# Kernel tuning notes

Hardware: AMD Instinct MI355X
Metric: run time of the kernel (lower is better)

The kernel has to match this reference:

```python
import jax, jax.numpy as jnp
import numpy as np

HIDDEN = 1024
HEADS = 16
HEAD_DIM = HIDDEN // HEADS


def setup_inputs() -> dict:
    key = jax.random.key(0)
    ks = jax.random.split(key, 11)
    B, S = 2, 2048
    s = 1.0 / np.sqrt(HIDDEN)
    return {
        "query": jax.random.normal(ks[0], (B, S, HIDDEN), jnp.float32),
        "key": jax.random.normal(ks[1], (B, S, HIDDEN), jnp.float32),
        "value": jax.random.normal(ks[2], (B, S, HIDDEN), jnp.float32),
        "Wq": jax.random.uniform(ks[3], (HIDDEN, HIDDEN), jnp.float32, -s, s),
        "bq": jax.random.uniform(ks[4], (HIDDEN,), jnp.float32, -s, s),
        "Wk": jax.random.uniform(ks[5], (HIDDEN, HIDDEN), jnp.float32, -s, s),
        "bk": jax.random.uniform(ks[6], (HIDDEN,), jnp.float32, -s, s),
        "Wv": jax.random.uniform(ks[7], (HIDDEN, HIDDEN), jnp.float32, -s, s),
        "bv": jax.random.uniform(ks[8], (HIDDEN,), jnp.float32, -s, s),
        "Wo": jax.random.uniform(ks[9], (HIDDEN, HIDDEN), jnp.float32, -s, s),
        "bo": jax.random.uniform(ks[10], (HIDDEN,), jnp.float32, -s, s),
    }


def reference(query, key, value, Wq, bq, Wk, bk, Wv, bv, Wo, bo):
    B, Sq, _ = query.shape
    Sk = key.shape[1]
    # projections (torch Linear: x @ W^T + b)
    Q = (query @ Wq.T + bq).reshape(B, Sq, HEADS, HEAD_DIM).transpose(0, 2, 1, 3)
    K = (key @ Wk.T + bk).reshape(B, Sk, HEADS, HEAD_DIM).transpose(0, 2, 1, 3)
    V = (value @ Wv.T + bv).reshape(B, Sk, HEADS, HEAD_DIM).transpose(0, 2, 1, 3)
    scale = jnp.sqrt(jnp.float32(HEAD_DIM))
    scores = jnp.einsum("bhqd,bhkd->bhqk", Q, K) / scale  # [B,H,Sq,Sk]
    # causal mask (is_causal=True, Sq>1)
    causal = jnp.tril(jnp.ones((Sq, Sk), dtype=bool))
    scores = jnp.where(causal[None, None], scores, -jnp.inf)
    attn = jax.nn.softmax(scores, axis=-1)
    out = jnp.einsum("bhqk,bhkd->bhqd", attn, V)
    out = out.transpose(0, 2, 1, 3).reshape(B, Sq, HIDDEN)
    return out @ Wo.T + bo
```

## Files before the change

### kernel.cpp

```cpp
#include <hip/hip_runtime.h>
#include <hip/hip_bf16.h>


typedef __attribute__((ext_vector_type(4))) float f32x4;
typedef __attribute__((ext_vector_type(8))) short bf16x8;
typedef unsigned short u16;

#define SEQ   2048
#define NH    16
#define HD    64
#define HID   1024
#define CEXP  0.1803368801f
#define MEG   1048576u

static __device__ __forceinline__ u16 f2bf(float f) {
  union { __hip_bfloat16 h; u16 u; } c;
  c.h = __float2bfloat16(f);
  return c.u;
}

static __device__ __forceinline__ int swz(int row, int col8) {
  return col8 ^ ((row & 7) << 3);
}

static __device__ __forceinline__ void gll16(const void* g, void* l) {
  __builtin_amdgcn_global_load_lds(
      (const __attribute__((address_space(1))) void*)g,
      (__attribute__((address_space(3))) void*)l, 16, 0, 0);
}

__global__ __launch_bounds__(256) void cvt_kernel(
    const float* __restrict__ Wq, const float* __restrict__ Wk,
    const float* __restrict__ Wv, const float* __restrict__ Wo,
    const float* __restrict__ q, const float* __restrict__ k,
    const float* __restrict__ v,
    u16* __restrict__ wsout, u16* __restrict__ dob) {
  const int y = blockIdx.y;
  const int c = y & 3;
  const float* src;
  u16* dst;
  if (y < 4) {
    src = (y == 0) ? Wq : (y == 1) ? Wk : (y == 2) ? Wv : Wo;
    dst = wsout + (size_t)y * MEG;
  } else if (y < 8) {
    src = q + (size_t)c * MEG;
    dst = wsout + 4u * MEG + (size_t)c * MEG;
  } else if (y < 12) {
    src = k + (size_t)c * MEG;
    dst = dob + (size_t)c * MEG;
  } else {
    src = v + (size_t)c * MEG;
    dst = dob + 4u * MEG + (size_t)c * MEG;
  }
  int i = (blockIdx.x * 256 + threadIdx.x) * 4;
  float4 f = *(const float4*)(src + i);
  ushort4 o;
  o.x = f2bf(f.x); o.y = f2bf(f.y); o.z = f2bf(f.z); o.w = f2bf(f.w);
  *(ushort4*)(dst + i) = o;
}

__global__ __launch_bounds__(256) void proj_kernel(
    const u16* __restrict__ Xq, const u16* __restrict__ Xk,
    const u16* __restrict__ Xv, const u16* __restrict__ Wc,
    const float* __restrict__ bq, const float* __restrict__ bk,
    const float* __restrict__ bvp,
    u16* __restrict__ Qo, u16* __restrict__ Ko, u16* __restrict__ Vto) {
  __shared__ u16 As[2][128 * 64];
  __shared__ u16 Bs[2][128 * 64];

  const int tid  = threadIdx.x;
  const int lane = tid & 63;
  const int wid  = tid >> 6;
  const int wm   = wid >> 1, wn = wid & 1;
  const int l15  = lane & 15;
  const int lhi  = lane >> 4;
  const int z    = blockIdx.z;
  const int bm   = blockIdx.x * 128;
  const int bn   = blockIdx.y * 128;

  const u16* X = (z == 0) ? Xq : (z == 1) ? Xk : Xv;
  const u16* W = Wc + (size_t)z * (HID * HID);
  const float* bias = (z == 0) ? bq : (z == 1) ? bk : bvp;

  f32x4 acc[4][4];
#pragma unroll
  for (int i = 0; i < 4; i++)
#pragma unroll
    for (int j = 0; j < 4; j++) acc[i][j] = (f32x4){0.f, 0.f, 0.f, 0.f};

  const int lrow  = lane >> 3;
  const int gcol8 = lane & 7;

#define PROJ_STAGE(buf, k0)                                                       \
  {                                                                               \
    _Pragma("unroll")                                                             \
    for (int c = 0; c < 4; c++) {                                                 \
      const int row  = c * 32 + wid * 8 + lrow;                                   \
      const int scol = (gcol8 ^ (row & 7)) * 8;      \
      gll16(X + (size_t)(bm + row) * HID + (k0) + scol,                           \
            (char*)&As[buf][0] + c * 4096 + wid * 1024);                          \
      gll16(W + (size_t)(bn + row) * HID + (k0) + scol,                           \
            (char*)&Bs[buf][0] + c * 4096 + wid * 1024);                          \
    }                                                                             \
  }

  PROJ_STAGE(0, 0);
  for (int t = 0; t < 16; t++) {
    __syncthreads();
    if (t < 15) PROJ_STAGE((t + 1) & 1, (t + 1) * 64);
    const u16* A = &As[t & 1][0];
    const u16* B = &Bs[t & 1][0];
#pragma unroll
    for (int ks = 0; ks < 2; ks++) {
      bf16x8 af[4], bfm[4];
#pragma unroll
      for (int i = 0; i < 4; i++) {
        const int row = wm * 64 + i * 16 + l15;
        af[i] = *(const bf16x8*)&A[row * 64 + swz(row, ks * 32 + lhi * 8)];
      }
#pragma unroll
      for (int j = 0; j < 4; j++) {
        const int row = wn * 64 + j * 16 + l15;
        bfm[j] = *(const bf16x8*)&B[row * 64 + swz(row, ks * 32 + lhi * 8)];
      }
#pragma unroll
      for (int i = 0; i < 4; i++)
#pragma unroll
        for (int j = 0; j < 4; j++)
          acc[i][j] = __builtin_amdgcn_mfma_f32_16x16x32_bf16(af[i], bfm[j], acc[i][j], 0, 0, 0);
    }
  }

  const int bb = bm >> 11;
#pragma unroll
  for (int j = 0; j < 4; j++) {
    const int n = bn + wn * 64 + j * 16 + l15;
    const float bv_ = bias[n];
    const int h = n >> 6, d = n & 63;
    if (z == 2) {
#pragma unroll
      for (int i = 0; i < 4; i++) {
        const int s0 = (bm + wm * 64 + i * 16 + lhi * 4) & 2047;
        ushort4 t;
        t.x = f2bf(acc[i][j][0] + bv_);
        t.y = f2bf(acc[i][j][1] + bv_);
        t.z = f2bf(acc[i][j][2] + bv_);
        t.w = f2bf(acc[i][j][3] + bv_);
        *(ushort4*)&Vto[((size_t)(bb * NH + h) * HD + d) * SEQ + s0] = t;
      }
    } else {
      u16* O = z ? Ko : Qo;
#pragma unroll
      for (int i = 0; i < 4; i++)
#pragma unroll
        for (int r = 0; r < 4; r++) {
          const int m = bm + wm * 64 + i * 16 + lhi * 4 + r;
          const int s = m & 2047;
          O[(((size_t)(bb * NH + h) * SEQ + s) << 6) + d] = f2bf(acc[i][j][r] + bv_);
        }
    }
  }
#undef PROJ_STAGE
}

__global__ __launch_bounds__(512) void attn_kernel(
    const u16* __restrict__ Q, const u16* __restrict__ K,
    const u16* __restrict__ Vt, u16* __restrict__ Aout) {
  __shared__ __align__(16) char pool[51200];

  const int tid  = threadIdx.x;
  const int lane = tid & 63;
  const int wid  = tid >> 6;
  const int rw   = wid & 3;
  const int g    = wid >> 2;
  const int l15  = lane & 15;
  const int lhi  = lane >> 4;

  const int flat = blockIdx.x;
  const int slot = flat >> 3;
  const int bh   = (flat & 7) * 4 + (slot & 3);
  const int qt   = 31 - (slot >> 2);
  const int b    = bh >> 4, h = bh & 15;
  const size_t base = (size_t)bh * SEQ * HD;

  u16* Ksh = (u16*)(pool + g * 8192);
  u16* Vsh = (u16*)(pool + 16384 + g * 8192);
  u16* Psh = (u16*)(pool + 32768 + wid * 2304);

  const int qrow = qt * 64 + rw * 16 + l15;
  bf16x8 aq[2];
  aq[0] = *(const bf16x8*)&Q[base + (size_t)qrow * HD + lhi * 8];
  aq[1] = *(const bf16x8*)&Q[base + (size_t)qrow * HD + 32 + lhi * 8];

  f32x4 o[4];
#pragma unroll
  for (int n = 0; n < 4; n++) o[n] = (f32x4){0.f, 0.f, 0.f, 0.f};
  float m_s = -1e30f, l_s = 0.f;

  const int gt   = tid & 255;
  const int srow = gt >> 2;
  const int sd   = (gt & 3) * 16;

  bf16x8 pk0, pk1, pv0, pv1;

#define ATTN_LOAD(kt_)                                                            \
  {                                                                               \
    const u16* kp = K + base + (size_t)((kt_) * 64 + srow) * HD + sd;             \
    pk0 = *(const bf16x8*)kp;                                                     \
    pk1 = *(const bf16x8*)(kp + 8);                                               \
    const u16* vp = Vt + base + (size_t)srow * SEQ + (kt_) * 64 + sd;             \
    pv0 = *(const bf16x8*)vp;                                                     \
    pv1 = *(const bf16x8*)(vp + 8);                                               \
  }

  if (g <= qt) ATTN_LOAD(g);

  const int nsteps = qt / 2 + 1;
  for (int it = 0; it < nsteps; ++it) {
    const int kt = 2 * it + g;
    const bool act = (kt <= qt);
    __syncthreads();
    if (act) {
      *(bf16x8*)&Ksh[srow * 64 + swz(srow, sd)]     = pk0;
      *(bf16x8*)&Ksh[srow * 64 + swz(srow, sd + 8)] = pk1;
      *(bf16x8*)&Vsh[srow * 64 + swz(srow, sd)]     = pv0;
      *(bf16x8*)&Vsh[srow * 64 + swz(srow, sd + 8)] = pv1;
    }
    const int ktn = kt + 2;
    if (ktn <= qt) ATTN_LOAD(ktn);
    __syncthreads();
    if (act) {
      f32x4 sc[4];
      __builtin_amdgcn_s_setprio(1);
#pragma unroll
      for (int n = 0; n < 4; n++) {
        sc[n] = (f32x4){0.f, 0.f, 0.f, 0.f};
#pragma unroll
        for (int ks = 0; ks < 2; ks++) {
          const int krow = n * 16 + l15;
          bf16x8 bk = *(const bf16x8*)&Ksh[krow * 64 + swz(krow, ks * 32 + lhi * 8)];
          sc[n] = __builtin_amdgcn_mfma_f32_16x16x32_bf16(bk, aq[ks], sc[n], 0, 0, 0);
        }
      }
      __builtin_amdgcn_s_setprio(0);
      if (kt == qt) {
#pragma unroll
        for (int n = 0; n < 4; n++)
#pragma unroll
          for (int r = 0; r < 4; r++)
            if (kt * 64 + n * 16 + lhi * 4 + r > qrow) sc[n][r] = -1e30f;
      }
      float mx = -1e30f;
#pragma unroll
      for (int n = 0; n < 4; n++)
        mx = fmaxf(mx, fmaxf(fmaxf(sc[n][0], sc[n][1]), fmaxf(sc[n][2], sc[n][3])));
      mx = fmaxf(mx, __shfl_xor(mx, 16, 64));
      mx = fmaxf(mx, __shfl_xor(mx, 32, 64));
      if (__any(mx > m_s + 64.0f)) {
        const float mnew = fmaxf(m_s, mx);
        const float fac = __builtin_amdgcn_exp2f((m_s - mnew) * CEXP);
        l_s *= fac;
        m_s = mnew;
        float facr[4];
#pragma unroll
        for (int r = 0; r < 4; r++) facr[r] = __shfl(fac, lhi * 4 + r, 64);
#pragma unroll
        for (int n = 0; n < 4; n++) {
          o[n][0] *= facr[0]; o[n][1] *= facr[1];
          o[n][2] *= facr[2]; o[n][3] *= facr[3];
        }
      }
      const float nmc = -m_s * CEXP;
      float ps = 0.f;
      u16 pb[4][4];
#pragma unroll
      for (int n = 0; n < 4; n++)
#pragma unroll
        for (int r = 0; r < 4; r++) {
          const float e = __builtin_amdgcn_exp2f(fmaf(sc[n][r], CEXP, nmc));
          ps += e;
          pb[n][r] = f2bf(e);
        }
      ps += __shfl_xor(ps, 16, 64);
      ps += __shfl_xor(ps, 32, 64);
      l_s += ps;
#pragma unroll
      for (int n = 0; n < 4; n++) {
        ushort4 t; t.x = pb[n][0]; t.y = pb[n][1]; t.z = pb[n][2]; t.w = pb[n][3];
        *(ushort4*)&Psh[l15 * 72 + n * 16 + lhi * 4] = t;
      }
      bf16x8 ap0 = *(const bf16x8*)&Psh[l15 * 72 + lhi * 8];
      bf16x8 ap1 = *(const bf16x8*)&Psh[l15 * 72 + 32 + lhi * 8];
      __builtin_amdgcn_s_setprio(1);
#pragma unroll
      for (int n = 0; n < 4; n++) {
        const int vrow = n * 16 + l15;
        bf16x8 bv0 = *(const bf16x8*)&Vsh[vrow * 64 + swz(vrow, lhi * 8)];
        bf16x8 bv1 = *(const bf16x8*)&Vsh[vrow * 64 + swz(vrow, 32 + lhi * 8)];
        o[n] = __builtin_amdgcn_mfma_f32_16x16x32_bf16(ap0, bv0, o[n], 0, 0, 0);
        o[n] = __builtin_amdgcn_mfma_f32_16x16x32_bf16(ap1, bv1, o[n], 0, 0, 0);
      }
      __builtin_amdgcn_s_setprio(0);
    }
  }
#undef ATTN_LOAD

  __syncthreads();
  float m_o[4], l_o[4];
#pragma unroll
  for (int r = 0; r < 4; r++) {
    m_o[r] = __shfl(m_s, lhi * 4 + r, 64);
    l_o[r] = __shfl(l_s, lhi * 4 + r, 64);
  }

  f32x4* comb = (f32x4*)pool;
  const int ci = (rw * 64 + lane) * 6;
  if (g == 0) {
#pragma unroll
    for (int n = 0; n < 4; n++) comb[ci + n] = o[n];
    comb[ci + 4] = (f32x4){m_o[0], m_o[1], m_o[2], m_o[3]};
    comb[ci + 5] = (f32x4){l_o[0], l_o[1], l_o[2], l_o[3]};
  }
  __syncthreads();
  if (g == 1) {
    f32x4 m0 = comb[ci + 4];
    f32x4 l0 = comb[ci + 5];
    float a0[4], a1[4], inv[4];
#pragma unroll
    for (int r = 0; r < 4; r++) {
      const float m = fmaxf(m0[r], m_o[r]);
      a0[r] = __builtin_amdgcn_exp2f((m0[r] - m) * CEXP);
      a1[r] = __builtin_amdgcn_exp2f((m_o[r] - m) * CEXP);
      inv[r] = 1.0f / (l0[r] * a0[r] + l_o[r] * a1[r]);
    }
#pragma unroll
    for (int n = 0; n < 4; n++) {
      f32x4 o0 = comb[ci + n];
#pragma unroll
      for (int r = 0; r < 4; r++) {
        const int rowg = qt * 64 + rw * 16 + lhi * 4 + r;
        const float val = (o0[r] * a0[r] + o[n][r] * a1[r]) * inv[r];
        Aout[(((size_t)(b * SEQ + rowg)) << 10) + h * 64 + n * 16 + l15] = f2bf(val);
      }
    }
  }
}

__global__ __launch_bounds__(256) void oproj_kernel(
    const u16* __restrict__ X, const u16* __restrict__ W,
    const float* __restrict__ bias, float* __restrict__ Out) {
  __shared__ u16 As[2][128 * 64];
  __shared__ u16 Bs[2][64 * 64];

  const int tid  = threadIdx.x;
  const int lane = tid & 63;
  const int wid  = tid >> 6;
  const int wm   = wid >> 1, wn = wid & 1;
  const int l15  = lane & 15;
  const int lhi  = lane >> 4;
  const int bm   = blockIdx.x * 128;
  const int bn   = blockIdx.y * 64;

  f32x4 acc[4][2];
#pragma unroll
  for (int i = 0; i < 4; i++)
#pragma unroll
    for (int j = 0; j < 2; j++) acc[i][j] = (f32x4){0.f, 0.f, 0.f, 0.f};

  const int lrow  = lane >> 3;
  const int gcol8 = lane & 7;

#define OPROJ_STAGE(buf, k0)                                                      \
  {                                                                               \
    _Pragma("unroll")                                                             \
    for (int c = 0; c < 4; c++) {                                                 \
      const int row  = c * 32 + wid * 8 + lrow;                                   \
      const int scol = (gcol8 ^ (row & 7)) * 8;                                   \
      gll16(X + (size_t)(bm + row) * HID + (k0) + scol,                           \
            (char*)&As[buf][0] + c * 4096 + wid * 1024);                          \
      if (c < 2)                                                                  \
        gll16(W + (size_t)(bn + row) * HID + (k0) + scol,                         \
              (char*)&Bs[buf][0] + c * 4096 + wid * 1024);                        \
    }                                                                             \
  }

  OPROJ_STAGE(0, 0);
  for (int t = 0; t < 16; t++) {
    __syncthreads();
    if (t < 15) OPROJ_STAGE((t + 1) & 1, (t + 1) * 64);
    const u16* A = &As[t & 1][0];
    const u16* B = &Bs[t & 1][0];
#pragma unroll
    for (int ks = 0; ks < 2; ks++) {
      bf16x8 af[4], bfm[2];
#pragma unroll
      for (int i = 0; i < 4; i++) {
        const int row = wm * 64 + i * 16 + l15;
        af[i] = *(const bf16x8*)&A[row * 64 + swz(row, ks * 32 + lhi * 8)];
      }
#pragma unroll
      for (int j = 0; j < 2; j++) {
        const int row = wn * 32 + j * 16 + l15;
        bfm[j] = *(const bf16x8*)&B[row * 64 + swz(row, ks * 32 + lhi * 8)];
      }
#pragma unroll
      for (int i = 0; i < 4; i++)
#pragma unroll
        for (int j = 0; j < 2; j++)
          acc[i][j] = __builtin_amdgcn_mfma_f32_16x16x32_bf16(af[i], bfm[j], acc[i][j], 0, 0, 0);
    }
  }
#undef OPROJ_STAGE

#pragma unroll
  for (int j = 0; j < 2; j++) {
    const int n = bn + wn * 32 + j * 16 + l15;
    const float bv_ = bias[n];
#pragma unroll
    for (int i = 0; i < 4; i++)
#pragma unroll
      for (int r = 0; r < 4; r++) {
        const int m = bm + wm * 64 + i * 16 + lhi * 4 + r;
        Out[(size_t)m * HID + n] = acc[i][j][r] + bv_;
      }
  }
}

extern "C" void kernel_launch(void* const* d_in, const int* in_sizes, int n_in,
                              void* d_out, int out_size, void* d_ws, size_t ws_size,
                              hipStream_t stream) {
  const float* q  = (const float*)d_in[0];
  const float* k  = (const float*)d_in[1];
  const float* v  = (const float*)d_in[2];
  const float* Wq = (const float*)d_in[3];
  const float* bq = (const float*)d_in[4];
  const float* Wk = (const float*)d_in[5];
  const float* bk = (const float*)d_in[6];
  const float* Wv = (const float*)d_in[7];
  const float* bv = (const float*)d_in[8];
  const float* Wo = (const float*)d_in[9];
  const float* bo = (const float*)d_in[10];

  u16* ws   = (u16*)d_ws;
  u16* wqkv = ws;
  u16* wob  = ws + 3u * MEG;
  u16* qb   = ws + 4u * MEG;
  u16* Qb   = ws + 8u * MEG;
  u16* Kb   = ws + 12u * MEG;
  u16* Vtb  = ws + 16u * MEG;
  u16* Ab   = qb;
  u16* kbf  = (u16*)d_out;
  u16* vbf  = (u16*)d_out + 4u * MEG;

  cvt_kernel<<<dim3(1024, 16), 256, 0, stream>>>(Wq, Wk, Wv, Wo, q, k, v, ws, kbf);

  proj_kernel<<<dim3(32, 8, 3), 256, 0, stream>>>(qb, kbf, vbf, wqkv, bq, bk, bv,
                                                  Qb, Kb, Vtb);

  attn_kernel<<<dim3(1024), 512, 0, stream>>>(Qb, Kb, Vtb, Ab);

  oproj_kernel<<<dim3(32, 16), 256, 0, stream>>>(Ab, wob, bo, (float*)d_out);
}
```

Before: 119.6 us.

## Replace __syncthreads with raw barriers and explicit partial vmcnt waits

After: 112.8 us. -5.8%, faster.

```diff
diff --git a/kernel.cpp b/kernel.cpp
--- a/kernel.cpp
+++ b/kernel.cpp
@@ -12,6 +12,9 @@
 #define HID   1024
 #define CEXP  0.1803368801f
 #define MEG   1048576u
+
+#define BAR()  __builtin_amdgcn_s_barrier()
+#define SCHED0() __builtin_amdgcn_sched_barrier(0)
 
 static __device__ __forceinline__ u16 f2bf(float f) {
   union { __hip_bfloat16 h; u16 u; } c;
@@ -106,8 +109,15 @@
 
   PROJ_STAGE(0, 0);
   for (int t = 0; t < 16; t++) {
-    __syncthreads();
-    if (t < 15) PROJ_STAGE((t + 1) & 1, (t + 1) * 64);
+    BAR();
+    if (t < 15) {
+      PROJ_STAGE((t + 1) & 1, (t + 1) * 64);
+      asm volatile("s_waitcnt vmcnt(8)" ::: "memory");
+    } else {
+      asm volatile("s_waitcnt vmcnt(0)" ::: "memory");
+    }
+    BAR();
+    SCHED0();
     const u16* A = &As[t & 1][0];
     const u16* B = &Bs[t & 1][0];
 #pragma unroll
@@ -130,6 +140,7 @@
           acc[i][j] = __builtin_amdgcn_mfma_f32_16x16x32_bf16(af[i], bfm[j], acc[i][j], 0, 0, 0);
     }
   }
+#undef PROJ_STAGE
 
   const int bb = bm >> 11;
 #pragma unroll
@@ -160,7 +171,6 @@
         }
     }
   }
-#undef PROJ_STAGE
 }
 
 __global__ __launch_bounds__(512) void attn_kernel(
@@ -219,7 +229,7 @@
   for (int it = 0; it < nsteps; ++it) {
     const int kt = 2 * it + g;
     const bool act = (kt <= qt);
-    __syncthreads();
+    BAR();
     if (act) {
       *(bf16x8*)&Ksh[srow * 64 + swz(srow, sd)]     = pk0;
       *(bf16x8*)&Ksh[srow * 64 + swz(srow, sd + 8)] = pk1;
@@ -228,7 +238,9 @@
     }
     const int ktn = kt + 2;
     if (ktn <= qt) ATTN_LOAD(ktn);
-    __syncthreads();
+    asm volatile("s_waitcnt lgkmcnt(0)" ::: "memory");
+    BAR();
+    SCHED0();
     if (act) {
       f32x4 sc[4];
       __builtin_amdgcn_s_setprio(1);
@@ -386,8 +398,15 @@
 
   OPROJ_STAGE(0, 0);
   for (int t = 0; t < 16; t++) {
-    __syncthreads();
-    if (t < 15) OPROJ_STAGE((t + 1) & 1, (t + 1) * 64);
+    BAR();
+    if (t < 15) {
+      OPROJ_STAGE((t + 1) & 1, (t + 1) * 64);
+      asm volatile("s_waitcnt vmcnt(6)" ::: "memory");
+    } else {
+      asm volatile("s_waitcnt vmcnt(0)" ::: "memory");
+    }
+    BAR();
+    SCHED0();
     const u16* A = &As[t & 1][0];
     const u16* B = &Bs[t & 1][0];
 #pragma unroll
```
